# Kernel optimization log

Hardware: AMD Instinct MI355X
Metric: run time of the kernel (lower is better)

The kernel has to match this reference:

```python
import jax, jax.numpy as jnp
import numpy as np

B, N, D, H_IMG, W_IMG = 1, 6, 128, 28, 60
HB, WB = 50, 50
HEADS, DH = 4, 32
INNER = HEADS * DH  # 128 == D
Q = HB * WB
NK = N * H_IMG * W_IMG


def _ln(x, w, b, eps=1e-5):
    m = jnp.mean(x, axis=-1, keepdims=True)
    v = jnp.var(x, axis=-1, keepdims=True)
    return (x - m) * jax.lax.rsqrt(v + eps) * w + b


def setup_inputs() -> dict:
    key = jax.random.key(0)
    ks = jax.random.split(key, 20)
    s = 0.02
    inp = {
        "q": jax.random.normal(ks[0], (B, D, HB, WB), jnp.float32),
        "k": jax.random.normal(ks[1], (B, N, D, H_IMG, W_IMG), jnp.float32),
        "v": jax.random.normal(ks[2], (B, N, D, H_IMG, W_IMG), jnp.float32),
        "W_logits": jax.random.uniform(ks[3], (B, Q, NK), jnp.float32),
        "vis_flat": jax.random.randint(ks[4], (B, Q, NK), 0, 2).astype(jnp.int32),
        "skip": jax.random.normal(ks[5], (B, D, HB, WB), jnp.float32),
        # LayerNorm params
        "qn_w": jnp.ones((D,), jnp.float32), "qn_b": jnp.zeros((D,), jnp.float32),
        "kn_w": jnp.ones((D,), jnp.float32), "kn_b": jnp.zeros((D,), jnp.float32),
        "vn_w": jnp.ones((D,), jnp.float32), "vn_b": jnp.zeros((D,), jnp.float32),
        "pre_w": jnp.ones((D,), jnp.float32), "pre_b": jnp.zeros((D,), jnp.float32),
        "post_w": jnp.ones((D,), jnp.float32), "post_b": jnp.zeros((D,), jnp.float32),
        # Linear params, stored [in, out]
        "wq": jax.random.normal(ks[6], (D, INNER), jnp.float32) * s,
        "bq": jnp.zeros((INNER,), jnp.float32),
        "wk": jax.random.normal(ks[7], (D, INNER), jnp.float32) * s,
        "bk": jnp.zeros((INNER,), jnp.float32),
        "wv": jax.random.normal(ks[8], (D, INNER), jnp.float32) * s,
        "bv": jnp.zeros((INNER,), jnp.float32),
        "wp": jax.random.normal(ks[9], (INNER, D), jnp.float32) * s,
        "bp": jnp.zeros((D,), jnp.float32),
        "w1": jax.random.normal(ks[10], (D, 2 * D), jnp.float32) * s,
        "b1": jnp.zeros((2 * D,), jnp.float32),
        "w2": jax.random.normal(ks[11], (2 * D, D), jnp.float32) * s,
        "b2": jnp.zeros((D,), jnp.float32),
    }
    return inp


def reference(q, k, v, W_logits, vis_flat, skip,
              qn_w, qn_b, kn_w, kn_b, vn_w, vn_b, pre_w, pre_b, post_w, post_b,
              wq, bq, wk, bk, wv, bv, wp, bp, w1, b1, w2, b2):
    b, d, Hb, Wb = q.shape
    _, n, _, hi, wi = k.shape
    Qn = Hb * Wb
    # b d H W -> b (H W) d ; b n d h w -> b (n h w) d
    qf = q.reshape(b, d, Qn).transpose(0, 2, 1)
    kf = k.transpose(0, 1, 3, 4, 2).reshape(b, n * hi * wi, d)
    vf = v.transpose(0, 1, 3, 4, 2).reshape(b, n * hi * wi, d)
    qf = _ln(qf, qn_w, qn_b)
    kf = _ln(kf, kn_w, kn_b)
    vf = _ln(vf, vn_w, vn_b)
    qh = (qf @ wq + bq).reshape(b, Qn, HEADS, DH).transpose(0, 2, 1, 3)
    kh = (kf @ wk + bk).reshape(b, -1, HEADS, DH).transpose(0, 2, 1, 3)
    vh = (vf @ wv + bv).reshape(b, -1, HEADS, DH).transpose(0, 2, 1, 3)
    scale = DH ** (-0.5)
    logits = jnp.einsum('bhqd,bhkd->bhqk', qh, kh) * scale  # [b,h,Q,NK]
    neg_inf = jnp.finfo(logits.dtype).min
    logits = jnp.where(vis_flat[:, None] == 0, neg_inf, logits)
    logits = logits * W_logits[:, None]  # multiplicative EAF weighting
    attn = jax.nn.softmax(logits, axis=-1)
    out = jnp.einsum('bhqk,bhkd->bhqd', attn, vh)
    out = out.transpose(0, 2, 1, 3).reshape(b, Qn, INNER)
    out = out @ wp + bp
    z = out + skip.reshape(b, d, Qn).transpose(0, 2, 1)
    z = _ln(z, pre_w, pre_b)
    z = z + (jax.nn.gelu(z @ w1 + b1, approximate=False) @ w2 + b2)
    z = _ln(z, post_w, post_b)
    return z.transpose(0, 2, 1).reshape(b, d, Hb, Wb)
```

## Files before the change

kernel.cpp:

```cpp
#include <hip/hip_runtime.h>
#include <hip/hip_bf16.h>
#include <math.h>

typedef short short8 __attribute__((ext_vector_type(8)));
typedef float floatx4 __attribute__((ext_vector_type(4)));
typedef int   intx4  __attribute__((ext_vector_type(4)));

#define D 128
#define Q 2500
#define QPAD 2560
#define NK 10080
#define NKPAD 10112
#define SPLITS 35
#define CPS 9
#define OPS 163904
#define LPS 10304
#define VBW 320
#define QSCALE 0.25501268426834347f
#define NEGBIG -3.0e38f

__device__ __forceinline__ unsigned short f2bf(float f) {
    unsigned u = __float_as_uint(f);
    unsigned r = (u + 0x7fffu + ((u >> 16) & 1u)) >> 16;
    return (unsigned short)r;
}
__device__ __forceinline__ unsigned pack2bf(float lo, float hi) {
    unsigned u0 = __float_as_uint(lo) + 0x8000u;
    unsigned u1 = __float_as_uint(hi) + 0x8000u;
    return (u0 >> 16) | (u1 & 0xffff0000u);
}
__device__ __forceinline__ float bflo(unsigned u) { return __uint_as_float(u << 16); }
__device__ __forceinline__ float bfhi(unsigned u) { return __uint_as_float(u & 0xffff0000u); }

__global__ __launch_bounds__(256) void pack_kernel(
    const int* __restrict__ vis, unsigned* __restrict__ vbits) {
    int row = blockIdx.x;
    int t = threadIdx.x;
    const int* src = vis + (size_t)row * NK;
    #pragma unroll 2
    for (int w = t; w < 315; w += 256) {
        unsigned bits = 0;
        const intx4* p = (const intx4*)(src + w * 32);
        #pragma unroll
        for (int g = 0; g < 8; g++) {
            intx4 v = p[g];
            #pragma unroll
            for (int j = 0; j < 4; j++) bits |= (v[j] ? 1u : 0u) << (g * 4 + j);
        }
        vbits[(size_t)row * VBW + w] = bits;
    }
}

__global__ __launch_bounds__(256) void prep_kernel(
    const float* __restrict__ qi, const float* __restrict__ ki, const float* __restrict__ vi,
    const float* __restrict__ qw, const float* __restrict__ qb_,
    const float* __restrict__ kw, const float* __restrict__ kb,
    const float* __restrict__ vw, const float* __restrict__ vb,
    unsigned short* __restrict__ xq, unsigned short* __restrict__ xk,
    unsigned short* __restrict__ xv,
    const float* __restrict__ wq, const float* __restrict__ wk,
    const float* __restrict__ wv, const float* __restrict__ wp,
    const float* __restrict__ w1, const float* __restrict__ w2,
    unsigned short* __restrict__ wqT, unsigned short* __restrict__ wkT,
    unsigned short* __restrict__ wvT, unsigned short* __restrict__ wpT,
    unsigned short* __restrict__ w1T, unsigned short* __restrict__ w2T) {
    int bid = blockIdx.x, t = threadIdx.x;
    if (bid >= 715) {
        int idx = (bid - 715) * 256 + t;
        if (idx < 49152) {
            int m = idx >> 14;
            int local = idx & 16383;
            int n = local >> 7, kk = local & 127;
            const float* w = (m == 0) ? wq : ((m == 1) ? wk : wv);
            unsigned short* o = (m == 0) ? wqT : ((m == 1) ? wkT : wvT);
            o[local] = f2bf(w[kk * 128 + n]);
        } else if (idx < 65536) {
            int local = idx - 49152;
            int n = local >> 7, kk = local & 127;
            wpT[local] = f2bf(wp[kk * 128 + n]);
        } else if (idx < 98304) {
            int local = idx - 65536;
            int n = local >> 7, kk = local & 127;
            w1T[local] = f2bf(w1[kk * 256 + n]);
        } else {
            int local = idx - 98304;
            int n = local >> 8, kk = local & 255;
            w2T[local] = f2bf(w2[kk * 128 + n]);
        }
        return;
    }
    __shared__ float lds2[32 * 132];
    const float* src; unsigned short* dst; const float *g, *b;
    int S, valid;
    if (bid < 79) {
        int p0 = bid * 32;
        src = qi + p0; S = Q; dst = xq + p0 * D; g = qw; b = qb_;
        valid = Q - p0; if (valid > 32) valid = 32;
    } else if (bid < 397) {
        int tt = bid - 79;
        int n = tt / 53, tile = tt - n * 53, r = tile * 32;
        src = ki + (size_t)(n * 128) * 1680 + r; S = 1680;
        dst = xk + (n * 1680 + r) * D; g = kw; b = kb;
        valid = 1680 - r; if (valid > 32) valid = 32;
    } else {
        int tt = bid - 397;
        int n = tt / 53, tile = tt - n * 53, r = tile * 32;
        src = vi + (size_t)(n * 128) * 1680 + r; S = 1680;
        dst = xv + (n * 1680 + r) * D; g = vw; b = vb;
        valid = 1680 - r; if (valid > 32) valid = 32;
    }
    #pragma unroll
    for (int pass = 0; pass < 4; pass++) {
        int s = pass * 256 + t;
        int d = s >> 3, ps = s & 7;
        floatx4 val = {0.f, 0.f, 0.f, 0.f};
        if (ps * 4 < valid) val = *(const floatx4*)(src + (size_t)d * S + ps * 4);
        #pragma unroll
        for (int j = 0; j < 4; j++) lds2[(ps * 4 + j) * 132 + d] = val[j];
    }
    __syncthreads();
    int lane = t & 63, wvx = t >> 6;
    int pos = wvx * 8 + (lane >> 3), l7 = lane & 7;
    floatx4 x4[4];
    #pragma unroll
    for (int k = 0; k < 4; k++) x4[k] = *(const floatx4*)(&lds2[pos * 132 + l7 * 16 + k * 4]);
    float s = 0.f, ss = 0.f;
    #pragma unroll
    for (int k = 0; k < 4; k++)
        #pragma unroll
        for (int j = 0; j < 4; j++) { s += x4[k][j]; ss += x4[k][j] * x4[k][j]; }
    #pragma unroll
    for (int m = 1; m <= 4; m <<= 1) { s += __shfl_xor(s, m, 64); ss += __shfl_xor(ss, m, 64); }
    float mean = s * (1.0f / 128.0f);
    float var = ss * (1.0f / 128.0f) - mean * mean;
    float rstd = rsqrtf(var + 1e-5f);
    short8 o1, o2;
    #pragma unroll
    for (int k = 0; k < 4; k++) {
        floatx4 g4 = *(const floatx4*)(g + l7 * 16 + k * 4);
        floatx4 b4 = *(const floatx4*)(b + l7 * 16 + k * 4);
        #pragma unroll
        for (int j = 0; j < 4; j++) {
            float o = (x4[k][j] - mean) * rstd * g4[j] + b4[j];
            if (k < 2) o1[k * 4 + j] = (short)f2bf(o);
            else o2[(k - 2) * 4 + j] = (short)f2bf(o);
        }
    }
    if (pos < valid) {
        *(short8*)(dst + pos * D + l7 * 16) = o1;
        *(short8*)(dst + pos * D + l7 * 16 + 8) = o2;
    }
}

__global__ __launch_bounds__(256) void proj_kernel(
    const unsigned short* __restrict__ xq, const unsigned short* __restrict__ xk,
    const unsigned short* __restrict__ xv,
    const unsigned short* __restrict__ wqT, const unsigned short* __restrict__ wkT,
    const unsigned short* __restrict__ wvT,
    const float* __restrict__ bq, const float* __restrict__ bk, const float* __restrict__ bv,
    unsigned short* __restrict__ qh, unsigned short* __restrict__ kh,
    unsigned short* __restrict__ vhT) {
    __shared__ short vlds[128 * 72];
    int bid = blockIdx.x;
    const unsigned short *src, *wT; const float* bias; int mb, mode; float scale;
    if (bid < 40)       { mode = 0; src = xq; wT = wqT; bias = bq; mb = bid * 64; scale = QSCALE; }
    else if (bid < 198) { mode = 1; src = xk; wT = wkT; bias = bk; mb = (bid - 40) * 64; scale = 1.0f; }
    else                { mode = 2; src = xv; wT = wvT; bias = bv; mb = (bid - 198) * 64; scale = 1.0f; }
    int t = threadIdx.x, wave = t >> 6, lane = t & 63;
    int l15 = lane & 15, quad = lane >> 4;
    int m0 = mb + wave * 16;
    floatx4 acc[8];
    #pragma unroll
    for (int i = 0; i < 8; i++) acc[i] = (floatx4){0.f, 0.f, 0.f, 0.f};
    #pragma unroll
    for (int kf = 0; kf < 4; kf++) {
        short8 A = *(const short8*)(src + (m0 + l15) * D + kf * 32 + quad * 8);
        #pragma unroll
        for (int nt = 0; nt < 8; nt++) {
            short8 Bv = *(const short8*)(wT + (nt * 16 + l15) * D + kf * 32 + quad * 8);
            acc[nt] = __builtin_amdgcn_mfma_f32_16x16x32_bf16(A, Bv, acc[nt], 0, 0, 0);
        }
    }
    if (mode != 2) {
        unsigned short* dst = (mode == 0) ? qh : kh;
        #pragma unroll
        for (int nt = 0; nt < 8; nt++) {
            float bb = bias[nt * 16 + l15];
            #pragma unroll
            for (int r = 0; r < 4; r++)
                dst[(m0 + quad * 4 + r) * D + nt * 16 + l15] = f2bf((acc[nt][r] + bb) * scale);
        }
    } else {
        #pragma unroll
        for (int nt = 0; nt < 8; nt++) {
            float bb = bias[nt * 16 + l15];
            #pragma unroll
            for (int r = 0; r < 4; r++)
                vlds[(nt * 16 + l15) * 72 + (wave * 16 + quad * 4 + r)] =
                    (short)f2bf(acc[nt][r] + bb);
        }
        __syncthreads();
        int pr = t & 31, dd = t >> 5;
        int sub = pr >> 4, i = pr & 15;
        #pragma unroll
        for (int pass = 0; pass < 16; pass++) {
            int d = pass * 8 + dd;
            unsigned lo = (unsigned short)vlds[d * 72 + sub * 32 + i];
            unsigned hi = (unsigned short)vlds[d * 72 + sub * 32 + 16 + i];
            *(unsigned*)(vhT + (size_t)d * NKPAD + mb + sub * 32 + 2 * i) = lo | (hi << 16);
        }
    }
}

template<int USEBITS>
__global__ __launch_bounds__(256, 3) void attn_kernel_t(
    const unsigned short* __restrict__ qh, const unsigned short* __restrict__ kh,
    const unsigned short* __restrict__ vhT,
    const float* __restrict__ Wl, const int* __restrict__ vis,
    const unsigned* __restrict__ vbits,
    unsigned* __restrict__ OpartU, float* __restrict__ lpart) {
    __shared__ short Kl[2][32 * 136];
    __shared__ short Vl[2][128 * 48];
    __shared__ unsigned Pl[4][16 * 18];
    int bid = blockIdx.x;
    int split = bid % SPLITS, qt = bid / SPLITS;
    int t = threadIdx.x, wave = t >> 6, lane = t & 63;
    int l15 = lane & 15, quad = lane >> 4;
    int qb = qt * 64 + wave * 16;
    int k00 = split * (CPS * 32);

    short8 qB[4];
    #pragma unroll
    for (int h = 0; h < 4; h++)
        qB[h] = *(const short8*)(qh + (size_t)(qb + l15) * D + h * 32 + quad * 8);

    int kr = t >> 3, ks = (t & 7) * 2;
    int vd = t >> 1, vs = (t & 1) * 2;
    const uint4* ksrc = (const uint4*)(kh + (size_t)(k00 + kr) * D + ks * 8);
    const uint4* vsrc = (const uint4*)(vhT + (size_t)vd * NKPAD + k00 + vs * 8);
    short* kdst = &Kl[0][kr * 136 + ks * 8];
    short* vdst = &Vl[0][vd * 48 + vs * 8];

    int wrow = qb + l15; if (wrow >= Q) wrow = Q - 1;
    const float* wp = Wl + (size_t)wrow * NK + k00 + quad * 4;
    const int*   vp = vis + (size_t)wrow * NK + k00 + quad * 4;
    const unsigned* vbp = vbits + (size_t)wrow * VBW + split * CPS;

    const floatx4 zf = {0.f, 0.f, 0.f, 0.f};
    floatx4 O[4][2];
    float lacc[4];
    #pragma unroll
    for (int h = 0; h < 4; h++) { O[h][0] = zf; O[h][1] = zf; lacc[h] = 0.f; }

    uint4 ka = ksrc[0], kb2 = ksrc[1];
    uint4 va = vsrc[0], vb2 = vsrc[1];
    floatx4 wc0 = *(const floatx4*)wp;
    floatx4 wc1 = *(const floatx4*)(wp + 16);
    intx4 vc0, vc1;
    unsigned vbc = 0;
    if constexpr (USEBITS) {
        vbc = vbp[0];
    } else {
        vc0 = *(const intx4*)vp;
        vc1 = *(const intx4*)(vp + 16);
    }
    *(uint4*)kdst = ka;       *(uint4*)(kdst + 8) = kb2;
    *(uint4*)vdst = va;       *(uint4*)(vdst + 8) = vb2;

    unsigned* pw = Pl[wave];
    #pragma unroll 1
    for (int c = 0; c < CPS; c++) {
        __syncthreads();
        int buf = c & 1;
        uint4 nka, nkb, nva, nvb;
        floatx4 wn0, wn1; intx4 vn0, vn1;
        unsigned vbn = 0;
        if (c + 1 < CPS) {
            const uint4* ks2 = ksrc + (size_t)(c + 1) * 512;
            const uint4* vs2 = vsrc + (size_t)(c + 1) * 4;
            nka = ks2[0]; nkb = ks2[1];
            nva = vs2[0]; nvb = vs2[1];
            wn0 = *(const floatx4*)(wp + (c + 1) * 32);
            wn1 = *(const floatx4*)(wp + (c + 1) * 32 + 16);
            if constexpr (USEBITS) {
                vbn = vbp[c + 1];
            } else {
                vn0 = *(const intx4*)(vp + (c + 1) * 32);
                vn1 = *(const intx4*)(vp + (c + 1) * 32 + 16);
            }
        }
        float a2[8], b2[8];
        if constexpr (USEBITS) {
            unsigned bq = vbc >> (quad * 4);
            #pragma unroll
            for (int r = 0; r < 4; r++) {
                bool m0 = (bq >> r) & 1u;
                bool m1 = (bq >> (16 + r)) & 1u;
                a2[r]     = m0 ? wc0[r] : 0.f;
                b2[r]     = m0 ? 0.f : wc0[r] * NEGBIG;
                a2[4 + r] = m1 ? wc1[r] : 0.f;
                b2[4 + r] = m1 ? 0.f : wc1[r] * NEGBIG;
            }
        } else {
            #pragma unroll
            for (int r = 0; r < 4; r++) {
                a2[r]     = vc0[r] ? wc0[r] : 0.f;
                b2[r]     = vc0[r] ? 0.f : wc0[r] * NEGBIG;
                a2[4 + r] = vc1[r] ? wc1[r] : 0.f;
                b2[4 + r] = vc1[r] ? 0.f : wc1[r] * NEGBIG;
            }
        }
        const short* Kb = Kl[buf];
        const short* Vb = Vl[buf];
        #pragma unroll
        for (int h = 0; h < 4; h++) {
            short8 kA0 = *(const short8*)(Kb + l15 * 136 + h * 32 + quad * 8);
            short8 kA1 = *(const short8*)(Kb + (16 + l15) * 136 + h * 32 + quad * 8);
            floatx4 S0 = __builtin_amdgcn_mfma_f32_16x16x32_bf16(kA0, qB[h], zf, 0, 0, 0);
            floatx4 S1 = __builtin_amdgcn_mfma_f32_16x16x32_bf16(kA1, qB[h], zf, 0, 0, 0);
            float p0[4], p1[4];
            #pragma unroll
            for (int r = 0; r < 4; r++) {
                p0[r] = exp2f(S0[r] * a2[r] + b2[r]);
                p1[r] = exp2f(S1[r] * a2[4 + r] + b2[4 + r]);
                lacc[h] += p0[r] + p1[r];
            }
            pw[(quad * 2) * 18 + l15]     = pack2bf(p0[0], p0[1]);
            pw[(quad * 2 + 1) * 18 + l15] = pack2bf(p0[2], p0[3]);
            pw[(8 + quad * 2) * 18 + l15]     = pack2bf(p1[0], p1[1]);
            pw[(8 + quad * 2 + 1) * 18 + l15] = pack2bf(p1[2], p1[3]);
            union { unsigned u[4]; short8 s8; } pb;
            #pragma unroll
            for (int jj = 0; jj < 4; jj++)
                pb.u[jj] = pw[(quad * 4 + jj) * 18 + l15];
            short8 vA0 = *(const short8*)(Vb + (h * 32 + l15) * 48 + quad * 8);
            short8 vA1 = *(const short8*)(Vb + (h * 32 + 16 + l15) * 48 + quad * 8);
            O[h][0] = __builtin_amdgcn_mfma_f32_16x16x32_bf16(vA0, pb.s8, O[h][0], 0, 0, 0);
            O[h][1] = __builtin_amdgcn_mfma_f32_16x16x32_bf16(vA1, pb.s8, O[h][1], 0, 0, 0);
        }
        if (c + 1 < CPS) {
            short* kd = buf ? kdst : (kdst + 32 * 136);
            short* vd2 = buf ? vdst : (vdst + 128 * 48);
            *(uint4*)kd = nka;       *(uint4*)(kd + 8) = nkb;
            *(uint4*)vd2 = nva;      *(uint4*)(vd2 + 8) = nvb;
            wc0 = wn0; wc1 = wn1;
            if constexpr (USEBITS) { vbc = vbn; }
            else { vc0 = vn0; vc1 = vn1; }
        }
    }

    int row = qb + l15;
    #pragma unroll
    for (int h = 0; h < 4; h++) {
        float lv = lacc[h];
        lv += __shfl_xor(lv, 16, 64);
        lv += __shfl_xor(lv, 32, 64);
        if (quad == 0) lpart[(size_t)split * LPS + row * 4 + h] = lv;
        #pragma unroll
        for (int tl = 0; tl < 2; tl++) {
            uint2 o2;
            o2.x = pack2bf(O[h][tl][0], O[h][tl][1]);
            o2.y = pack2bf(O[h][tl][2], O[h][tl][3]);
            *(uint2*)(OpartU + (size_t)split * OPS + ((size_t)row * 4 + h) * 16 + tl * 8 + quad * 2) = o2;
        }
    }
}

__global__ __launch_bounds__(128) void combine_kernel(
    const unsigned* __restrict__ Opart, const float* __restrict__ lpart,
    unsigned* __restrict__ A1u) {
    int tid = blockIdx.x * 128 + threadIdx.x;
    int sl = tid & 3, he = (tid >> 2) & 3, grow = tid >> 4;
    float lsum = 0.f;
    #pragma unroll 7
    for (int sp = 0; sp < SPLITS; sp++) lsum += lpart[(size_t)sp * LPS + grow * 4 + he];
    float inv = 1.0f / fmaxf(lsum, 1e-30f);
    size_t base = ((size_t)grow * 4 + he) * 16 + sl * 4;
    float a0 = 0.f, a1 = 0.f, a2 = 0.f, a3 = 0.f, a4 = 0.f, a5 = 0.f, a6 = 0.f, a7 = 0.f;
    #pragma unroll 7
    for (int sp = 0; sp < SPLITS; sp++) {
        uint4 u = *(const uint4*)(Opart + (size_t)sp * OPS + base);
        a0 += bflo(u.x); a1 += bfhi(u.x);
        a2 += bflo(u.y); a3 += bfhi(u.y);
        a4 += bflo(u.z); a5 += bfhi(u.z);
        a6 += bflo(u.w); a7 += bfhi(u.w);
    }
    uint4 o;
    o.x = pack2bf(a0 * inv, a1 * inv);
    o.y = pack2bf(a2 * inv, a3 * inv);
    o.z = pack2bf(a4 * inv, a5 * inv);
    o.w = pack2bf(a6 * inv, a7 * inv);
    *(uint4*)(A1u + (size_t)grow * 64 + he * 16 + sl * 4) = o;
}

__global__ __launch_bounds__(256) void mlp_kernel(
    const unsigned short* __restrict__ A1,
    const unsigned short* __restrict__ wpT,
    const float* __restrict__ bp, const float* __restrict__ skip,
    const float* __restrict__ pre_w, const float* __restrict__ pre_b,
    const unsigned short* __restrict__ w1T, const float* __restrict__ b1,
    const unsigned short* __restrict__ w2T, const float* __restrict__ b2,
    const float* __restrict__ post_w, const float* __restrict__ post_b,
    float* __restrict__ out) {
    __shared__ __align__(16) char smem[51200];
    short* Z1 = (short*)smem;
    short* H1 = (short*)(smem + 17408);
    float* Zout = (float*)smem;

    int qb = blockIdx.x * 64;
    int t = threadIdx.x, wave = t >> 6, lane = t & 63;
    int l15 = lane & 15, quad = lane >> 4;
    int m0 = wave * 16;

    floatx4 z[8];
    #pragma unroll
    for (int i = 0; i < 8; i++) z[i] = (floatx4){0.f, 0.f, 0.f, 0.f};
    #pragma unroll
    for (int kf = 0; kf < 4; kf++) {
        short8 A = *(const short8*)(A1 + (size_t)(qb + m0 + l15) * 128 + kf * 32 + quad * 8);
        #pragma unroll
        for (int nt = 0; nt < 8; nt++) {
            short8 Bv = *(const short8*)(wpT + (nt * 16 + l15) * D + kf * 32 + quad * 8);
            z[nt] = __builtin_amdgcn_mfma_f32_16x16x32_bf16(A, Bv, z[nt], 0, 0, 0);
        }
    }
    float Zv[8][4];
    #pragma unroll
    for (int nt = 0; nt < 8; nt++) {
        int n = nt * 16 + l15;
        float bb = bp[n];
        #pragma unroll
        for (int r = 0; r < 4; r++) {
            int q = qb + m0 + quad * 4 + r;
            int qc = q < Q ? q : (Q - 1);
            Zv[nt][r] = z[nt][r] + bb + skip[n * Q + qc];
        }
    }
    float Zn[8][4];
    {
        #pragma unroll
        for (int r = 0; r < 4; r++) {
            float s1 = 0.f, s2 = 0.f;
            #pragma unroll
            for (int nt = 0; nt < 8; nt++) { s1 += Zv[nt][r]; s2 += Zv[nt][r] * Zv[nt][r]; }
            #pragma unroll
            for (int m = 1; m <= 8; m <<= 1) { s1 += __shfl_xor(s1, m, 64); s2 += __shfl_xor(s2, m, 64); }
            float mean = s1 * (1.0f / 128.0f);
            float var = s2 * (1.0f / 128.0f) - mean * mean;
            float rstd = rsqrtf(var + 1e-5f);
            #pragma unroll
            for (int nt = 0; nt < 8; nt++) Zn[nt][r] = (Zv[nt][r] - mean) * rstd;
        }
        #pragma unroll
        for (int nt = 0; nt < 8; nt++) {
            int n = nt * 16 + l15;
            float g = pre_w[n], be = pre_b[n];
            #pragma unroll
            for (int r = 0; r < 4; r++) {
                Zn[nt][r] = Zn[nt][r] * g + be;
                Z1[(m0 + quad * 4 + r) * 136 + n] = (short)f2bf(Zn[nt][r]);
            }
        }
    }
    {
        floatx4 h2[16];
        #pragma unroll
        for (int i = 0; i < 16; i++) h2[i] = (floatx4){0.f, 0.f, 0.f, 0.f};
        #pragma unroll
        for (int kf = 0; kf < 4; kf++) {
            short8 A = *(const short8*)(Z1 + (m0 + l15) * 136 + kf * 32 + quad * 8);
            #pragma unroll
            for (int nt = 0; nt < 16; nt++) {
                short8 Bv = *(const short8*)(w1T + (nt * 16 + l15) * D + kf * 32 + quad * 8);
                h2[nt] = __builtin_amdgcn_mfma_f32_16x16x32_bf16(A, Bv, h2[nt], 0, 0, 0);
            }
        }
        #pragma unroll
        for (int nt = 0; nt < 16; nt++) {
            int n = nt * 16 + l15;
            float bb = b1[n];
            #pragma unroll
            for (int r = 0; r < 4; r++) {
                float x = h2[nt][r] + bb;
                float gl = 0.5f * x * (1.0f + erff(x * 0.70710678118654752f));
                H1[(m0 + quad * 4 + r) * 264 + n] = (short)f2bf(gl);
            }
        }
    }
    floatx4 o3[8];
    #pragma unroll
    for (int i = 0; i < 8; i++) o3[i] = (floatx4){0.f, 0.f, 0.f, 0.f};
    #pragma unroll
    for (int kf = 0; kf < 8; kf++) {
        short8 A = *(const short8*)(H1 + (m0 + l15) * 264 + kf * 32 + quad * 8);
        #pragma unroll
        for (int nt = 0; nt < 8; nt++) {
            short8 Bv = *(const short8*)(w2T + (nt * 16 + l15) * 256 + kf * 32 + quad * 8);
            o3[nt] = __builtin_amdgcn_mfma_f32_16x16x32_bf16(A, Bv, o3[nt], 0, 0, 0);
        }
    }
    float Z2[8][4];
    #pragma unroll
    for (int nt = 0; nt < 8; nt++) {
        int n = nt * 16 + l15;
        float bb = b2[n];
        #pragma unroll
        for (int r = 0; r < 4; r++) Z2[nt][r] = Zn[nt][r] + o3[nt][r] + bb;
    }
    float Zo[8][4];
    {
        #pragma unroll
        for (int r = 0; r < 4; r++) {
            float s1 = 0.f, s2 = 0.f;
            #pragma unroll
            for (int nt = 0; nt < 8; nt++) { s1 += Z2[nt][r]; s2 += Z2[nt][r] * Z2[nt][r]; }
            #pragma unroll
            for (int m = 1; m <= 8; m <<= 1) { s1 += __shfl_xor(s1, m, 64); s2 += __shfl_xor(s2, m, 64); }
            float mean = s1 * (1.0f / 128.0f);
            float var = s2 * (1.0f / 128.0f) - mean * mean;
            float rstd = rsqrtf(var + 1e-5f);
            #pragma unroll
            for (int nt = 0; nt < 8; nt++) Zo[nt][r] = (Z2[nt][r] - mean) * rstd;
        }
        #pragma unroll
        for (int nt = 0; nt < 8; nt++) {
            int n = nt * 16 + l15;
            float g = post_w[n], be = post_b[n];
            #pragma unroll
            for (int r = 0; r < 4; r++) Zo[nt][r] = Zo[nt][r] * g + be;
        }
    }
    __syncthreads();
    #pragma unroll
    for (int nt = 0; nt < 8; nt++)
        #pragma unroll
        for (int r = 0; r < 4; r++)
            Zout[(nt * 16 + l15) * 65 + m0 + quad * 4 + r] = Zo[nt][r];
    __syncthreads();
    {
        int pl = t & 63;
        int q = qb + pl;
        if (q < Q) {
            #pragma unroll
            for (int it = 0; it < 32; it++) {
                int n = it * 4 + (t >> 6);
                out[n * Q + q] = Zout[n * 65 + pl];
            }
        }
    }
}

extern "C" void kernel_launch(void* const* d_in, const int* in_sizes, int n_in,
                              void* d_out, int out_size, void* d_ws, size_t ws_size,
                              hipStream_t stream) {
    (void)in_sizes; (void)n_in; (void)out_size;
    const float* q      = (const float*)d_in[0];
    const float* k      = (const float*)d_in[1];
    const float* v      = (const float*)d_in[2];
    const float* Wl     = (const float*)d_in[3];
    const int*   vis    = (const int*)  d_in[4];
    const float* skip   = (const float*)d_in[5];
    const float* qn_w   = (const float*)d_in[6];
    const float* qn_b   = (const float*)d_in[7];
    const float* kn_w   = (const float*)d_in[8];
    const float* kn_b   = (const float*)d_in[9];
    const float* vn_w   = (const float*)d_in[10];
    const float* vn_b   = (const float*)d_in[11];
    const float* pre_w  = (const float*)d_in[12];
    const float* pre_b  = (const float*)d_in[13];
    const float* post_w = (const float*)d_in[14];
    const float* post_b = (const float*)d_in[15];
    const float* wq     = (const float*)d_in[16];
    const float* bq     = (const float*)d_in[17];
    const float* wk     = (const float*)d_in[18];
    const float* bk     = (const float*)d_in[19];
    const float* wv     = (const float*)d_in[20];
    const float* bv     = (const float*)d_in[21];
    const float* wp     = (const float*)d_in[22];
    const float* bp     = (const float*)d_in[23];
    const float* w1     = (const float*)d_in[24];
    const float* b1     = (const float*)d_in[25];
    const float* w2     = (const float*)d_in[26];
    const float* b2     = (const float*)d_in[27];
    float* out = (float*)d_out;

    char* ws = (char*)d_ws;
    unsigned short* xq  = (unsigned short*)(ws + 0);
    unsigned short* xk  = (unsigned short*)(ws + 655360);
    unsigned short* xv  = (unsigned short*)(ws + 3244032);
    unsigned short* qh  = (unsigned short*)(ws + 5832704);
    unsigned short* kh  = (unsigned short*)(ws + 6488064);
    unsigned short* vhT = (unsigned short*)(ws + 9076736);
    unsigned short* wqT = (unsigned short*)(ws + 11665408);
    unsigned short* wkT = (unsigned short*)(ws + 11698176);
    unsigned short* wvT = (unsigned short*)(ws + 11730944);
    unsigned short* wpT = (unsigned short*)(ws + 11763712);
    unsigned short* w1T = (unsigned short*)(ws + 11796480);
    unsigned short* w2T = (unsigned short*)(ws + 11862016);
    unsigned* OpartU    = (unsigned*)(ws + 11927552);
    float* lpart        = (float*)(ws + 34874112);
    unsigned* vbits     = (unsigned*)(ws + 36316672);
    unsigned* A1u       = (unsigned*)(ws + 0);

    const bool usebits = (ws_size == 0) || (ws_size >= 39520000ull);

    if (usebits)
        pack_kernel<<<dim3(2500), dim3(256), 0, stream>>>(vis, vbits);
    prep_kernel<<<dim3(1227), dim3(256), 0, stream>>>(
        q, k, v, qn_w, qn_b, kn_w, kn_b, vn_w, vn_b, xq, xk, xv,
        wq, wk, wv, wp, w1, w2, wqT, wkT, wvT, wpT, w1T, w2T);
    proj_kernel<<<dim3(356), dim3(256), 0, stream>>>(xq, xk, xv, wqT, wkT, wvT, bq, bk, bv,
                                                     qh, kh, vhT);
    if (usebits)
        attn_kernel_t<1><<<dim3(40 * SPLITS), dim3(256), 0, stream>>>(
            qh, kh, vhT, Wl, vis, vbits, OpartU, lpart);
    else
        attn_kernel_t<0><<<dim3(40 * SPLITS), dim3(256), 0, stream>>>(
            qh, kh, vhT, Wl, vis, vbits, OpartU, lpart);
    combine_kernel<<<dim3(320), dim3(128), 0, stream>>>(OpartU, lpart, A1u);
    mlp_kernel<<<dim3(40), dim3(256), 0, stream>>>((const unsigned short*)A1u, wpT, bp, skip,
                                                   pre_w, pre_b, w1T, b1, w2T, b2,
                                                   post_w, post_b, out);
}
```

Measured before the change: 372.1 us.

## Fold mask packing into prep kernel and rebalance attention splits

Moves the visibility-bit packing into extra blocks of the prep kernel, which saves one launch and lets packing overlap with the LayerNorm prep work. Changes the attention key split from 35 splits of 9 chunks to 19 splits of 17 chunks, adding a per-split chunk bound so the last split stops at the end of the keys. V's shared-memory row stride shrinks from 48 to 40 shorts. Fewer splits cut the partial-output traffic and combine work but also cut the number of blocks, and the new stride may raise LDS bank conflicts.

```diff
diff --git a/kernel.cpp b/kernel.cpp
--- a/kernel.cpp
+++ b/kernel.cpp
@@ -11,11 +11,12 @@
 #define QPAD 2560
 #define NK 10080
 #define NKPAD 10112
-#define SPLITS 35
-#define CPS 9
+#define SPLITS 19
+#define CPS 17
 #define OPS 163904
 #define LPS 10304
 #define VBW 320
+#define VROW 40
 #define QSCALE 0.25501268426834347f
 #define NEGBIG -3.0e38f
 
@@ -31,25 +32,6 @@
 }
 __device__ __forceinline__ float bflo(unsigned u) { return __uint_as_float(u << 16); }
 __device__ __forceinline__ float bfhi(unsigned u) { return __uint_as_float(u & 0xffff0000u); }
-
-__global__ __launch_bounds__(256) void pack_kernel(
-    const int* __restrict__ vis, unsigned* __restrict__ vbits) {
-    int row = blockIdx.x;
-    int t = threadIdx.x;
-    const int* src = vis + (size_t)row * NK;
-    #pragma unroll 2
-    for (int w = t; w < 315; w += 256) {
-        unsigned bits = 0;
-        const intx4* p = (const intx4*)(src + w * 32);
-        #pragma unroll
-        for (int g = 0; g < 8; g++) {
-            intx4 v = p[g];
-            #pragma unroll
-            for (int j = 0; j < 4; j++) bits |= (v[j] ? 1u : 0u) << (g * 4 + j);
-        }
-        vbits[(size_t)row * VBW + w] = bits;
-    }
-}
 
 __global__ __launch_bounds__(256) void prep_kernel(
     const float* __restrict__ qi, const float* __restrict__ ki, const float* __restrict__ vi,
@@ -63,8 +45,26 @@
     const float* __restrict__ w1, const float* __restrict__ w2,
     unsigned short* __restrict__ wqT, unsigned short* __restrict__ wkT,
     unsigned short* __restrict__ wvT, unsigned short* __restrict__ wpT,
-    unsigned short* __restrict__ w1T, unsigned short* __restrict__ w2T) {
+    unsigned short* __restrict__ w1T, unsigned short* __restrict__ w2T,
+    const int* __restrict__ vis, unsigned* __restrict__ vbits) {
     int bid = blockIdx.x, t = threadIdx.x;
+    if (bid >= 1227) {
+        int row = bid - 1227;
+        const int* src = vis + (size_t)row * NK;
+        #pragma unroll 2
+        for (int w = t; w < 315; w += 256) {
+            unsigned bits = 0;
+            const intx4* p = (const intx4*)(src + w * 32);
+            #pragma unroll
+            for (int g = 0; g < 8; g++) {
+                intx4 v = p[g];
+                #pragma unroll
+                for (int j = 0; j < 4; j++) bits |= (v[j] ? 1u : 0u) << (g * 4 + j);
+            }
+            vbits[(size_t)row * VBW + w] = bits;
+        }
+        return;
+    }
     if (bid >= 715) {
         int idx = (bid - 715) * 256 + t;
         if (idx < 49152) {
@@ -220,7 +220,7 @@
     const unsigned* __restrict__ vbits,
     unsigned* __restrict__ OpartU, float* __restrict__ lpart) {
     __shared__ short Kl[2][32 * 136];
-    __shared__ short Vl[2][128 * 48];
+    __shared__ short Vl[2][128 * VROW];
     __shared__ unsigned Pl[4][16 * 18];
     int bid = blockIdx.x;
     int split = bid % SPLITS, qt = bid / SPLITS;
@@ -228,6 +228,7 @@
     int l15 = lane & 15, quad = lane >> 4;
     int qb = qt * 64 + wave * 16;
     int k00 = split * (CPS * 32);
+    int cmax = (NK - k00) >> 5; if (cmax > CPS) cmax = CPS;
 
     short8 qB[4];
     #pragma unroll
@@ -239,7 +240,7 @@
     const uint4* ksrc = (const uint4*)(kh + (size_t)(k00 + kr) * D + ks * 8);
     const uint4* vsrc = (const uint4*)(vhT + (size_t)vd * NKPAD + k00 + vs * 8);
     short* kdst = &Kl[0][kr * 136 + ks * 8];
-    short* vdst = &Vl[0][vd * 48 + vs * 8];
+    short* vdst = &Vl[0][vd * VROW + vs * 8];
 
     int wrow = qb + l15; if (wrow >= Q) wrow = Q - 1;
     const float* wp = Wl + (size_t)wrow * NK + k00 + quad * 4;
@@ -269,13 +270,13 @@
 
     unsigned* pw = Pl[wave];
     #pragma unroll 1
-    for (int c = 0; c < CPS; c++) {
+    for (int c = 0; c < cmax; c++) {
         __syncthreads();
         int buf = c & 1;
         uint4 nka, nkb, nva, nvb;
         floatx4 wn0, wn1; intx4 vn0, vn1;
         unsigned vbn = 0;
-        if (c + 1 < CPS) {
+        if (c + 1 < cmax) {
             const uint4* ks2 = ksrc + (size_t)(c + 1) * 512;
             const uint4* vs2 = vsrc + (size_t)(c + 1) * 4;
             nka = ks2[0]; nkb = ks2[1];
@@ -333,14 +334,14 @@
             #pragma unroll
             for (int jj = 0; jj < 4; jj++)
                 pb.u[jj] = pw[(quad * 4 + jj) * 18 + l15];
-            short8 vA0 = *(const short8*)(Vb + (h * 32 + l15) * 48 + quad * 8);
-            short8 vA1 = *(const short8*)(Vb + (h * 32 + 16 + l15) * 48 + quad * 8);
+            short8 vA0 = *(const short8*)(Vb + (h * 32 + l15) * VROW + quad * 8);
+            short8 vA1 = *(const short8*)(Vb + (h * 32 + 16 + l15) * VROW + quad * 8);
             O[h][0] = __builtin_amdgcn_mfma_f32_16x16x32_bf16(vA0, pb.s8, O[h][0], 0, 0, 0);
             O[h][1] = __builtin_amdgcn_mfma_f32_16x16x32_bf16(vA1, pb.s8, O[h][1], 0, 0, 0);
         }
-        if (c + 1 < CPS) {
+        if (c + 1 < cmax) {
             short* kd = buf ? kdst : (kdst + 32 * 136);
-            short* vd2 = buf ? vdst : (vdst + 128 * 48);
+            short* vd2 = buf ? vdst : (vdst + 128 * VROW);
             *(uint4*)kd = nka;       *(uint4*)(kd + 8) = nkb;
             *(uint4*)vd2 = nva;      *(uint4*)(vd2 + 8) = nvb;
             wc0 = wn0; wc1 = wn1;
@@ -372,12 +373,12 @@
     int tid = blockIdx.x * 128 + threadIdx.x;
     int sl = tid & 3, he = (tid >> 2) & 3, grow = tid >> 4;
     float lsum = 0.f;
-    #pragma unroll 7
+    #pragma unroll 5
     for (int sp = 0; sp < SPLITS; sp++) lsum += lpart[(size_t)sp * LPS + grow * 4 + he];
     float inv = 1.0f / fmaxf(lsum, 1e-30f);
     size_t base = ((size_t)grow * 4 + he) * 16 + sl * 4;
     float a0 = 0.f, a1 = 0.f, a2 = 0.f, a3 = 0.f, a4 = 0.f, a5 = 0.f, a6 = 0.f, a7 = 0.f;
-    #pragma unroll 7
+    #pragma unroll 5
     for (int sp = 0; sp < SPLITS; sp++) {
         uint4 u = *(const uint4*)(Opart + (size_t)sp * OPS + base);
         a0 += bflo(u.x); a1 += bfhi(u.x);
@@ -604,11 +605,9 @@
 
     const bool usebits = (ws_size == 0) || (ws_size >= 39520000ull);
 
-    if (usebits)
-        pack_kernel<<<dim3(2500), dim3(256), 0, stream>>>(vis, vbits);
-    prep_kernel<<<dim3(1227), dim3(256), 0, stream>>>(
+    prep_kernel<<<dim3(usebits ? 3727 : 1227), dim3(256), 0, stream>>>(
         q, k, v, qn_w, qn_b, kn_w, kn_b, vn_w, vn_b, xq, xk, xv,
-        wq, wk, wv, wp, w1, w2, wqT, wkT, wvT, wpT, w1T, w2T);
+        wq, wk, wv, wp, w1, w2, wqT, wkT, wvT, wpT, w1T, w2T, vis, vbits);
     proj_kernel<<<dim3(356), dim3(256), 0, stream>>>(xq, xk, xv, wqT, wkT, wvT, bq, bk, bv,
                                                      qh, kh, vhT);
     if (usebits)
```

Measured after the change: 364.5 us. 1.02x faster.
